# Optimization experiments

Hardware: AMD Instinct MI355X
Metric: run time of the kernel (lower is better)

The kernel has to match this reference:

```python
import jax, jax.numpy as jnp
import numpy as np

POOL_SIZES = (1, 3, 6, 8)
EPS = 1e-5


def conv1x1(x, W, b):
    # x: [b, cin, h, w], W: [cout, cin], b: [cout]
    return jnp.einsum('bchw,oc->bohw', x, W) + b[None, :, None, None]


def ppm(x):
    # x: [b, c, h, w] -> [b, c, S] with S = sum(p*p); H,W divisible by each p
    b, c, h, w = x.shape
    outs = []
    for p in POOL_SIZES:
        pooled = x.reshape(b, c, p, h // p, p, w // p).mean(axis=(3, 5))
        outs.append(pooled.reshape(b, c, p * p))
    return jnp.concatenate(outs, axis=-1)


def setup_inputs() -> dict:
    key = jax.random.key(0)
    ks = jax.random.split(key, 8)
    B, Cin, H, W = 4, 512, 120, 120
    Ck, Cv, Cout = 256, 256, 512
    x = jax.random.normal(ks[0], (B, Cin, H, W), dtype=jnp.float32)
    sc = lambda cin: 1.0 / np.sqrt(cin)
    Wk = jax.random.normal(ks[1], (Ck, Cin), dtype=jnp.float32) * sc(Cin)
    bk = jnp.zeros((Ck,), jnp.float32)
    gamma = jnp.ones((Ck,), jnp.float32)
    beta = jnp.zeros((Ck,), jnp.float32)
    mean = jax.random.normal(ks[2], (Ck,), dtype=jnp.float32) * 0.1
    var = jax.random.uniform(ks[3], (Ck,), dtype=jnp.float32, minval=0.5, maxval=1.5)
    Wv = jax.random.normal(ks[4], (Cv, Cin), dtype=jnp.float32) * sc(Cin)
    bv = jnp.zeros((Cv,), jnp.float32)
    # original inits Conv_Out to zero; use random weights for a nontrivial baseline
    Wo = jax.random.normal(ks[5], (Cout, Cv), dtype=jnp.float32) * sc(Cv)
    bo = jnp.zeros((Cout,), jnp.float32)
    return {'x': x, 'Wk': Wk, 'bk': bk, 'gamma': gamma, 'beta': beta,
            'mean': mean, 'var': var, 'Wv': Wv, 'bv': bv, 'Wo': Wo, 'bo': bo}


def reference(x, Wk, bk, gamma, beta, mean, var, Wv, bv, Wo, bo):
    b, _, h, w = x.shape
    ck = Wk.shape[0]
    cv = Wv.shape[0]
    # shared Conv_Key / Conv_Query: conv1x1 -> BN (inference) -> ReLU
    kq = conv1x1(x, Wk, bk)
    inv = gamma / jnp.sqrt(var + EPS)
    kq = jax.nn.relu(kq * inv[None, :, None, None] + (beta - mean * inv)[None, :, None, None])
    value = ppm(conv1x1(x, Wv, bv)).transpose(0, 2, 1)      # [b, S, cv]
    key = ppm(kq)                                            # [b, ck, S]
    query = kq.reshape(b, ck, h * w).transpose(0, 2, 1)      # [b, hw, ck]
    scores = jnp.einsum('bnc,bcs->bns', query, key) * (ck ** -0.5)
    attn = jax.nn.softmax(scores, axis=-1)                   # [b, hw, S]
    agg = jnp.einsum('bns,bsv->bnv', attn, value)            # [b, hw, cv]
    agg = agg.transpose(0, 2, 1).reshape(b, cv, h, w)
    return conv1x1(agg, Wo, bo)
```

## Files before the change

kernel.cpp:

```cpp
#include <hip/hip_runtime.h>
#include <cstdint>
#include <cstddef>

#define HW 14400
#define WIDTH 120
#define S_TOT 110

typedef unsigned short u16;
typedef __attribute__((ext_vector_type(8))) short bf16x8;
typedef __attribute__((ext_vector_type(4))) float f32x4;

__device__ __forceinline__ u16 f2bf(float x) {
  unsigned u = __float_as_uint(x);
  unsigned r = (u + 0x7fffu + ((u >> 16) & 1u)) >> 16;
  return (u16)r;
}
__device__ __forceinline__ float bf2f(u16 h) {
  return __uint_as_float((unsigned)h << 16);
}

__device__ __forceinline__ void async16(void* lds, const void* g) {
  __builtin_amdgcn_global_load_lds(
      (const __attribute__((address_space(1))) void*)g,
      (__attribute__((address_space(3))) void*)lds, 16, 0, 0);
}

__global__ __launch_bounds__(256) void pool_kernel(const float* __restrict__ in,
                                                   float* __restrict__ outp) {
  __shared__ float part[576];
  const float* plane = in + (size_t)blockIdx.x * HW;
  int t = threadIdx.x;
  for (int bb = t; bb < 576; bb += 256) {
    int by = bb / 24, bx = bb % 24;
    const float* p0 = plane + (by * 5) * WIDTH + bx * 5;
    float s = 0.f;
#pragma unroll
    for (int yy = 0; yy < 5; ++yy)
#pragma unroll
      for (int xx = 0; xx < 5; ++xx) s += p0[yy * WIDTH + xx];
    part[bb] = s;
  }
  __syncthreads();
  if (t < S_TOT) {
    float s = 0.f;
    if (t == 0) {
      for (int i = 0; i < 576; ++i) s += part[i];
      s *= (1.f / 14400.f);
    } else if (t < 10) {
      int idx = t - 1, i = idx / 3, j = idx % 3;
      for (int a = 0; a < 8; ++a)
        for (int c = 0; c < 8; ++c) s += part[(i * 8 + a) * 24 + (j * 8 + c)];
      s *= (1.f / 1600.f);
    } else if (t < 46) {
      int idx = t - 10, i = idx / 6, j = idx % 6;
      for (int a = 0; a < 4; ++a)
        for (int c = 0; c < 4; ++c) s += part[(i * 4 + a) * 24 + (j * 4 + c)];
      s *= (1.f / 400.f);
    } else {
      int idx = t - 46, i = idx / 8, j = idx % 8;
      for (int a = 0; a < 3; ++a)
        for (int c = 0; c < 3; ++c) s += part[(i * 3 + a) * 24 + (j * 3 + c)];
      s *= (1.f / 225.f);
    }
    outp[(size_t)blockIdx.x * S_TOT + t] = s;
  }
}

__global__ __launch_bounds__(256) void convert_w(const float* __restrict__ in,
                                                 u16* __restrict__ hi,
                                                 u16* __restrict__ lo, int n) {
  int i = blockIdx.x * 256 + threadIdx.x;
  if (i < n) {
    float v = in[i];
    u16 h = f2bf(v);
    hi[i] = h;
    lo[i] = f2bf(v - bf2f(h));
  }
}

template <int CIN>
__global__ __launch_bounds__(256) void convert_t(const float* __restrict__ X,
                                                 u16* __restrict__ xth,
                                                 u16* __restrict__ xtl) {
  __shared__ float ls[64][65];
  int b = blockIdx.z;
  int n0 = blockIdx.x * 64, k0 = blockIdx.y * 64;
  int t = threadIdx.x;
  int rt = t >> 4, c4 = (t & 15) * 4;
#pragma unroll
  for (int rr = 0; rr < 4; ++rr) {
    int kk = rr * 16 + rt;
    float4 v = *(const float4*)&X[((size_t)(b * CIN + k0 + kk)) * HW + n0 + c4];
    ls[kk][c4] = v.x; ls[kk][c4 + 1] = v.y; ls[kk][c4 + 2] = v.z; ls[kk][c4 + 3] = v.w;
  }
  __syncthreads();
#pragma unroll
  for (int rr = 0; rr < 4; ++rr) {
    int nn = rr * 16 + rt;
    float v0 = ls[c4 + 0][nn], v1 = ls[c4 + 1][nn], v2 = ls[c4 + 2][nn], v3 = ls[c4 + 3][nn];
    ushort4 oh, ol;
    oh.x = f2bf(v0); ol.x = f2bf(v0 - bf2f(oh.x));
    oh.y = f2bf(v1); ol.y = f2bf(v1 - bf2f(oh.y));
    oh.z = f2bf(v2); ol.z = f2bf(v2 - bf2f(oh.z));
    oh.w = f2bf(v3); ol.w = f2bf(v3 - bf2f(oh.w));
    size_t idx = ((size_t)(b * HW + n0 + nn)) * CIN + k0 + c4;
    *(ushort4*)&xth[idx] = oh;
    *(ushort4*)&xtl[idx] = ol;
  }
}

template <int K, int M_TOT, bool BNRELU>
__global__ __launch_bounds__(512, 2) void gemm_mfma(
    const u16* __restrict__ Ah, const u16* __restrict__ Al,
    const u16* __restrict__ Bh, const u16* __restrict__ Bl,
    float* __restrict__ C,
    const float* __restrict__ p0, const float* __restrict__ p1,
    const float* __restrict__ p2, const float* __restrict__ p3,
    const float* __restrict__ p4) {
  constexpr int NSTEP = K / 32;
  __shared__ alignas(16) u16 sA[3][16][512];
  __shared__ alignas(16) u16 sB[3][24][512];

  int t = threadIdx.x, w = t >> 6, l = t & 63;
  int wm = w >> 2, wn = w & 3;
  int b = blockIdx.z;
  int n0 = blockIdx.x * 192;
  int m0 = blockIdx.y * 128;

  int fr = l & 15, fkc = l >> 4;
  const size_t bOff = (size_t)b * HW;

  auto stage = [&](int ks, int slot) {
    int k0 = ks * 32;
#pragma unroll
    for (int c = 0; c < 5; ++c) {
      int i = w * 5 + c;
      const u16* g;
      u16* d;
      if (i < 8) {
        g = Ah + (size_t)(m0 + i * 16 + fr) * K + k0 + fkc * 8;
        d = &sA[slot][i][0];
      } else if (i < 16) {
        g = Al + (size_t)(m0 + (i - 8) * 16 + fr) * K + k0 + fkc * 8;
        d = &sA[slot][i][0];
      } else if (i < 28) {
        g = Bh + (bOff + n0 + (i - 16) * 16 + fr) * (size_t)K + k0 + fkc * 8;
        d = &sB[slot][i - 16][0];
      } else {
        g = Bl + (bOff + n0 + (i - 28) * 16 + fr) * (size_t)K + k0 + fkc * 8;
        d = &sB[slot][i - 16][0];
      }
      async16(d, g);
    }
  };

  f32x4 acc[4][3];
#pragma unroll
  for (int i = 0; i < 4; ++i)
#pragma unroll
    for (int j = 0; j < 3; ++j) acc[i][j] = (f32x4){0.f, 0.f, 0.f, 0.f};

  stage(0, 0);
  stage(1, 1);

  for (int ks = 0; ks < NSTEP; ++ks) {
    if (ks + 1 < NSTEP)
      asm volatile("s_waitcnt vmcnt(5)" ::: "memory");
    else
      asm volatile("s_waitcnt vmcnt(0)" ::: "memory");
    __builtin_amdgcn_s_barrier();
    __builtin_amdgcn_sched_barrier(0);

    if (ks + 2 < NSTEP) stage(ks + 2, (ks + 2) % 3);

    int cur = ks % 3;
    bf16x8 bh[3], bl[3];
#pragma unroll
    for (int nt = 0; nt < 3; ++nt) {
      bh[nt] = *(const bf16x8*)&sB[cur][wn * 3 + nt][l * 8];
      bl[nt] = *(const bf16x8*)&sB[cur][12 + wn * 3 + nt][l * 8];
    }
    bf16x8 ah[4], al[4];
#pragma unroll
    for (int mt = 0; mt < 4; ++mt) {
      ah[mt] = *(const bf16x8*)&sA[cur][wm * 4 + mt][l * 8];
      al[mt] = *(const bf16x8*)&sA[cur][8 + wm * 4 + mt][l * 8];
    }
    __builtin_amdgcn_s_setprio(1);
#pragma unroll
    for (int mt = 0; mt < 4; ++mt)
#pragma unroll
      for (int nt = 0; nt < 3; ++nt) {
        acc[mt][nt] = __builtin_amdgcn_mfma_f32_16x16x32_bf16(ah[mt], bh[nt], acc[mt][nt], 0, 0, 0);
        acc[mt][nt] = __builtin_amdgcn_mfma_f32_16x16x32_bf16(ah[mt], bl[nt], acc[mt][nt], 0, 0, 0);
        acc[mt][nt] = __builtin_amdgcn_mfma_f32_16x16x32_bf16(al[mt], bh[nt], acc[mt][nt], 0, 0, 0);
      }
    __builtin_amdgcn_s_setprio(0);
  }

#pragma unroll
  for (int mt = 0; mt < 4; ++mt) {
    int mb = m0 + (wm * 4 + mt) * 16 + (l >> 4) * 4;
    float iv[4], ad[4];
    if (BNRELU) {
      float4 g0 = *(const float4*)&p0[mb];
      float4 g1 = *(const float4*)&p1[mb];
      float4 g2 = *(const float4*)&p2[mb];
      float4 g3 = *(const float4*)&p3[mb];
      float4 g4 = *(const float4*)&p4[mb];
      iv[0] = g1.x * rsqrtf(g4.x + 1e-5f);
      iv[1] = g1.y * rsqrtf(g4.y + 1e-5f);
      iv[2] = g1.z * rsqrtf(g4.z + 1e-5f);
      iv[3] = g1.w * rsqrtf(g4.w + 1e-5f);
      ad[0] = (g0.x - g3.x) * iv[0] + g2.x;
      ad[1] = (g0.y - g3.y) * iv[1] + g2.y;
      ad[2] = (g0.z - g3.z) * iv[2] + g2.z;
      ad[3] = (g0.w - g3.w) * iv[3] + g2.w;
    } else {
      float4 g0 = *(const float4*)&p0[mb];
      ad[0] = g0.x; ad[1] = g0.y; ad[2] = g0.z; ad[3] = g0.w;
    }
#pragma unroll
    for (int nt = 0; nt < 3; ++nt) {
      int n = n0 + (wn * 3 + nt) * 16 + fr;
#pragma unroll
      for (int r = 0; r < 4; ++r) {
        float v = acc[mt][nt][r];
        if (BNRELU)
          v = fmaxf(v * iv[r] + ad[r], 0.f);
        else
          v = v + ad[r];
        C[((size_t)(b * M_TOT) + mb + r) * HW + n] = v;
      }
    }
  }
}

__global__ __launch_bounds__(256) void value_kernel(
    const float* __restrict__ Wv, const float* __restrict__ xp,
    const float* __restrict__ bv, u16* __restrict__ vth,
    u16* __restrict__ vtl) {
  int b = blockIdx.x >> 7, s = blockIdx.x & 127;
  int t = threadIdx.x;
  size_t o = ((size_t)(b * 256 + t)) * 128 + s;
  if (s >= S_TOT) { vth[o] = 0; vtl[o] = 0; return; }
  __shared__ float xs[512];
  for (int i = t; i < 512; i += 256) xs[i] = xp[((size_t)b * 512 + i) * S_TOT + s];
  __syncthreads();
  float accv = 0.f;
  const float* wv = Wv + (size_t)t * 512;
  for (int k = 0; k < 512; k += 4) {
    float4 w4 = *(const float4*)&wv[k];
    accv += w4.x * xs[k] + w4.y * xs[k + 1] + w4.z * xs[k + 2] + w4.w * xs[k + 3];
  }
  accv += bv[t];
  u16 h = f2bf(accv);
  vth[o] = h;
  vtl[o] = f2bf(accv - bf2f(h));
}

__global__ __launch_bounds__(256) void convert_key(const float* __restrict__ keyp,
                                                   u16* __restrict__ kth,
                                                   u16* __restrict__ ktl) {
  int b = blockIdx.x;
  int t = threadIdx.x;
  for (int i = t; i < 128 * 256; i += 256) {
    int s = i >> 8, c = i & 255;
    float v = (s < S_TOT) ? keyp[((size_t)(b * 256 + c)) * S_TOT + s] : 0.f;
    u16 h = f2bf(v);
    size_t o = ((size_t)(b * 128 + s)) * 256 + c;
    kth[o] = h;
    ktl[o] = f2bf(v - bf2f(h));
  }
}

__global__ __launch_bounds__(256) void attn_mfma(
    const u16* __restrict__ qh, const u16* __restrict__ ql,
    const u16* __restrict__ kh, const u16* __restrict__ kl,
    const u16* __restrict__ vh, const u16* __restrict__ vl,
    u16* __restrict__ aggh, u16* __restrict__ aggl) {
  __shared__ alignas(16) u16 lds[17408];
  int b = blockIdx.y, pix0 = blockIdx.x * 64;
  int t = threadIdx.x, w = t >> 6, l = t & 63;
  int fr = l & 15, q = l >> 4;

  const u16* kbase_h = kh + (size_t)b * 128 * 256;
  const u16* kbase_l = kl + (size_t)b * 128 * 256;

  f32x4 acc[8];
#pragma unroll
  for (int st = 0; st < 8; ++st) acc[st] = (f32x4){0.f, 0.f, 0.f, 0.f};

  const u16* qbh = qh + ((size_t)(b * HW + pix0 + w * 16 + fr)) * 256 + q * 8;
  const u16* qbl = ql + ((size_t)(b * HW + pix0 + w * 16 + fr)) * 256 + q * 8;

  auto stageK = [&](int ks, int buf) {
    int c0 = ks * 32;
#pragma unroll
    for (int j = 0; j < 4; ++j) {
      int i = t + j * 256;
      int half = i >> 9;
      int idx = i & 511;
      int st = idx >> 6, ll = idx & 63;
      const u16* src = (half ? kbase_l : kbase_h) +
                       (st * 16 + (ll & 15)) * 256 + c0 + (ll >> 4) * 8;
      async16(&lds[buf * 8192 + half * 4096 + idx * 8], src);
    }
  };

  stageK(0, 0);
  for (int ks = 0; ks < 8; ++ks) {
    __syncthreads();
    if (ks < 7) stageK(ks + 1, (ks + 1) & 1);
    bf16x8 ah = *(const bf16x8*)(qbh + ks * 32);
    bf16x8 al = *(const bf16x8*)(qbl + ks * 32);
    const u16* kb = &lds[(ks & 1) * 8192 + l * 8];
#pragma unroll
    for (int st = 0; st < 8; ++st) {
      bf16x8 bh = *(const bf16x8*)(kb + st * 512);
      bf16x8 bl = *(const bf16x8*)(kb + 4096 + st * 512);
      acc[st] = __builtin_amdgcn_mfma_f32_16x16x32_bf16(ah, bh, acc[st], 0, 0, 0);
      acc[st] = __builtin_amdgcn_mfma_f32_16x16x32_bf16(ah, bl, acc[st], 0, 0, 0);
      acc[st] = __builtin_amdgcn_mfma_f32_16x16x32_bf16(al, bh, acc[st], 0, 0, 0);
    }
  }

#pragma unroll
  for (int st = 0; st < 8; ++st)
#pragma unroll
    for (int r = 0; r < 4; ++r) acc[st][r] *= 0.0625f;
  if (fr >= 14) {
#pragma unroll
    for (int r = 0; r < 4; ++r) acc[6][r] = -1e30f;
  }
#pragma unroll
  for (int r = 0; r < 4; ++r) acc[7][r] = -1e30f;

#pragma unroll
  for (int r = 0; r < 4; ++r) {
    float m = -1e30f;
#pragma unroll
    for (int st = 0; st < 8; ++st) m = fmaxf(m, acc[st][r]);
    m = fmaxf(m, __shfl_xor(m, 1));
    m = fmaxf(m, __shfl_xor(m, 2));
    m = fmaxf(m, __shfl_xor(m, 4));
    m = fmaxf(m, __shfl_xor(m, 8));
    float s = 0.f;
#pragma unroll
    for (int st = 0; st < 8; ++st) {
      float e = __expf(acc[st][r] - m);
      acc[st][r] = e;
      s += e;
    }
    s += __shfl_xor(s, 1);
    s += __shfl_xor(s, 2);
    s += __shfl_xor(s, 4);
    s += __shfl_xor(s, 8);
    float inv = 1.f / s;
#pragma unroll
    for (int st = 0; st < 8; ++st) acc[st][r] *= inv;
  }

  __syncthreads();

  int prow = w * 16 + q * 4;
#pragma unroll
  for (int st = 0; st < 8; ++st) {
    int s = st * 16 + fr;
#pragma unroll
    for (int r = 0; r < 4; ++r) {
      float v = acc[st][r];
      u16 h = f2bf(v);
      lds[(prow + r) * 136 + s] = h;
      lds[8704 + (prow + r) * 136 + s] = f2bf(v - bf2f(h));
    }
  }
  __syncthreads();

  f32x4 oacc[4][4];
#pragma unroll
  for (int nt = 0; nt < 4; ++nt)
#pragma unroll
    for (int pt = 0; pt < 4; ++pt) oacc[nt][pt] = (f32x4){0.f, 0.f, 0.f, 0.f};

  const u16* vbh = vh + ((size_t)(b * 256 + w * 64 + fr)) * 128 + q * 8;
  const u16* vbl = vl + ((size_t)(b * 256 + w * 64 + fr)) * 128 + q * 8;

#pragma unroll
  for (int kc = 0; kc < 4; ++kc) {
    bf16x8 ph[4], pl[4];
#pragma unroll
    for (int pt = 0; pt < 4; ++pt) {
      ph[pt] = *(const bf16x8*)&lds[(pt * 16 + fr) * 136 + kc * 32 + q * 8];
      pl[pt] = *(const bf16x8*)&lds[8704 + (pt * 16 + fr) * 136 + kc * 32 + q * 8];
    }
#pragma unroll
    for (int nt = 0; nt < 4; ++nt) {
      bf16x8 a_h = *(const bf16x8*)(vbh + (size_t)nt * 16 * 128 + kc * 32);
      bf16x8 a_l = *(const bf16x8*)(vbl + (size_t)nt * 16 * 128 + kc * 32);
#pragma unroll
      for (int pt = 0; pt < 4; ++pt) {
        oacc[nt][pt] = __builtin_amdgcn_mfma_f32_16x16x32_bf16(a_h, ph[pt], oacc[nt][pt], 0, 0, 0);
        oacc[nt][pt] = __builtin_amdgcn_mfma_f32_16x16x32_bf16(a_h, pl[pt], oacc[nt][pt], 0, 0, 0);
        oacc[nt][pt] = __builtin_amdgcn_mfma_f32_16x16x32_bf16(a_l, ph[pt], oacc[nt][pt], 0, 0, 0);
      }
    }
  }

#pragma unroll
  for (int nt = 0; nt < 4; ++nt) {
#pragma unroll
    for (int pt = 0; pt < 4; ++pt) {
      ushort4 oh, ol;
      float v0 = oacc[nt][pt][0], v1 = oacc[nt][pt][1];
      float v2 = oacc[nt][pt][2], v3 = oacc[nt][pt][3];
      oh.x = f2bf(v0); ol.x = f2bf(v0 - bf2f(oh.x));
      oh.y = f2bf(v1); ol.y = f2bf(v1 - bf2f(oh.y));
      oh.z = f2bf(v2); ol.z = f2bf(v2 - bf2f(oh.z));
      oh.w = f2bf(v3); ol.w = f2bf(v3 - bf2f(oh.w));
      size_t o = ((size_t)(b * HW + pix0 + pt * 16 + fr)) * 256 + (w * 4 + nt) * 16 + q * 4;
      *(ushort4*)&aggh[o] = oh;
      *(ushort4*)&aggl[o] = ol;
    }
  }
}

extern "C" void kernel_launch(void* const* d_in, const int* in_sizes, int n_in,
                              void* d_out, int out_size, void* d_ws, size_t ws_size,
                              hipStream_t stream) {
  (void)in_sizes; (void)n_in; (void)out_size; (void)ws_size;
  const float* x     = (const float*)d_in[0];
  const float* Wk    = (const float*)d_in[1];
  const float* bk    = (const float*)d_in[2];
  const float* gamma = (const float*)d_in[3];
  const float* beta  = (const float*)d_in[4];
  const float* mean  = (const float*)d_in[5];
  const float* var   = (const float*)d_in[6];
  const float* Wv    = (const float*)d_in[7];
  const float* bv    = (const float*)d_in[8];
  const float* Wo    = (const float*)d_in[9];
  const float* bo    = (const float*)d_in[10];
  float* out = (float*)d_out;

  char* p = (char*)d_ws;
  float* kq = (float*)p;      p += (size_t)14745600 * 4;
  u16* xth = (u16*)p;         p += (size_t)29491200 * 2;
  u16* xtl = (u16*)p;         p += (size_t)29491200 * 2;
  u16* wkh = (u16*)p;         p += 131072 * 2;
  u16* wkl = (u16*)p;         p += 131072 * 2;
  u16* woh = (u16*)p;         p += 131072 * 2;
  u16* wol = (u16*)p;         p += 131072 * 2;
  float* xp = (float*)p;      p += (size_t)4 * 512 * 110 * 4;
  float* keyp = (float*)p;    p += (size_t)4 * 256 * 110 * 4;
  u16* vth = (u16*)p;         p += (size_t)4 * 256 * 128 * 2;
  u16* vtl = (u16*)p;         p += (size_t)4 * 256 * 128 * 2;
  u16* kth = (u16*)p;         p += (size_t)4 * 128 * 256 * 2;
  u16* ktl = (u16*)p;         p += (size_t)4 * 128 * 256 * 2;
  u16* aggh = xth;
  u16* kqth = xth + (size_t)14745600;
  u16* aggl = xtl;
  u16* kqtl = xtl + (size_t)14745600;

  convert_w<<<512, 256, 0, stream>>>(Wk, wkh, wkl, 256 * 512);
  convert_w<<<512, 256, 0, stream>>>(Wo, woh, wol, 512 * 256);
  convert_t<512><<<dim3(225, 8, 4), 256, 0, stream>>>(x, xth, xtl);
  pool_kernel<<<dim3(4 * 512), dim3(256), 0, stream>>>(x, xp);
  value_kernel<<<dim3(4 * 128), dim3(256), 0, stream>>>(Wv, xp, bv, vth, vtl);
  gemm_mfma<512, 256, true><<<dim3(75, 2, 4), 512, 0, stream>>>(
      wkh, wkl, xth, xtl, kq, bk, gamma, beta, mean, var);
  convert_t<256><<<dim3(225, 4, 4), 256, 0, stream>>>(kq, kqth, kqtl);
  pool_kernel<<<dim3(4 * 256), dim3(256), 0, stream>>>(kq, keyp);
  convert_key<<<dim3(4), dim3(256), 0, stream>>>(keyp, kth, ktl);
  attn_mfma<<<dim3(225, 4), 256, 0, stream>>>(kqth, kqtl, kth, ktl, vth, vtl,
                                              aggh, aggl);
  gemm_mfma<256, 512, false><<<dim3(75, 4, 4), 512, 0, stream>>>(
      woh, wol, aggh, aggl, out, bo, nullptr, nullptr, nullptr, nullptr);
}
```

Before: 560.0 us.

## Fuse kq transpose/bf16 split into key GEMM epilogue; separable pooling sums

The BN+ReLU key GEMM epilogue now also writes the transposed bf16 hi/lo split of kq through a padded LDS staging buffer, which removes the separate convert_t pass over kq when the workspace is large enough. Shared memory is merged into one flat array so the epilogue can reuse it after a barrier. The pool kernel first computes 5-row column sums and then sums 5 columns, cutting redundant global loads. The fused path needs about 59 MB more workspace and falls back to the old kernel if that is not available; the extra epilogue stores may add register pressure and stall the GEMM tail.

```diff
diff --git a/kernel.cpp b/kernel.cpp
--- a/kernel.cpp
+++ b/kernel.cpp
@@ -27,18 +27,20 @@
 
 __global__ __launch_bounds__(256) void pool_kernel(const float* __restrict__ in,
                                                    float* __restrict__ outp) {
+  __shared__ float colsum[2880];
   __shared__ float part[576];
   const float* plane = in + (size_t)blockIdx.x * HW;
   int t = threadIdx.x;
+  for (int i = t; i < 2880; i += 256) {
+    int by = i / 120, x = i - by * 120;
+    const float* p0 = plane + (by * 5) * WIDTH + x;
+    colsum[i] = p0[0] + p0[WIDTH] + p0[2 * WIDTH] + p0[3 * WIDTH] + p0[4 * WIDTH];
+  }
+  __syncthreads();
   for (int bb = t; bb < 576; bb += 256) {
-    int by = bb / 24, bx = bb % 24;
-    const float* p0 = plane + (by * 5) * WIDTH + bx * 5;
-    float s = 0.f;
-#pragma unroll
-    for (int yy = 0; yy < 5; ++yy)
-#pragma unroll
-      for (int xx = 0; xx < 5; ++xx) s += p0[yy * WIDTH + xx];
-    part[bb] = s;
+    int by = bb / 24, bx = bb - by * 24;
+    const float* c = &colsum[by * 120 + bx * 5];
+    part[bb] = c[0] + c[1] + c[2] + c[3] + c[4];
   }
   __syncthreads();
   if (t < S_TOT) {
@@ -116,10 +118,10 @@
     float* __restrict__ C,
     const float* __restrict__ p0, const float* __restrict__ p1,
     const float* __restrict__ p2, const float* __restrict__ p3,
-    const float* __restrict__ p4) {
+    const float* __restrict__ p4,
+    u16* __restrict__ Th, u16* __restrict__ Tl) {
   constexpr int NSTEP = K / 32;
-  __shared__ alignas(16) u16 sA[3][16][512];
-  __shared__ alignas(16) u16 sB[3][24][512];
+  __shared__ alignas(16) u16 smem[61440];
 
   int t = threadIdx.x, w = t >> 6, l = t & 63;
   int wm = w >> 2, wn = w & 3;
@@ -139,16 +141,16 @@
       u16* d;
       if (i < 8) {
         g = Ah + (size_t)(m0 + i * 16 + fr) * K + k0 + fkc * 8;
-        d = &sA[slot][i][0];
+        d = &smem[slot * 8192 + i * 512];
       } else if (i < 16) {
         g = Al + (size_t)(m0 + (i - 8) * 16 + fr) * K + k0 + fkc * 8;
-        d = &sA[slot][i][0];
+        d = &smem[slot * 8192 + i * 512];
       } else if (i < 28) {
         g = Bh + (bOff + n0 + (i - 16) * 16 + fr) * (size_t)K + k0 + fkc * 8;
-        d = &sB[slot][i - 16][0];
+        d = &smem[24576 + slot * 12288 + (i - 16) * 512];
       } else {
         g = Bl + (bOff + n0 + (i - 28) * 16 + fr) * (size_t)K + k0 + fkc * 8;
-        d = &sB[slot][i - 16][0];
+        d = &smem[24576 + slot * 12288 + (i - 16) * 512];
       }
       async16(d, g);
     }
@@ -177,14 +179,14 @@
     bf16x8 bh[3], bl[3];
 #pragma unroll
     for (int nt = 0; nt < 3; ++nt) {
-      bh[nt] = *(const bf16x8*)&sB[cur][wn * 3 + nt][l * 8];
-      bl[nt] = *(const bf16x8*)&sB[cur][12 + wn * 3 + nt][l * 8];
+      bh[nt] = *(const bf16x8*)&smem[24576 + cur * 12288 + (wn * 3 + nt) * 512 + l * 8];
+      bl[nt] = *(const bf16x8*)&smem[24576 + cur * 12288 + (12 + wn * 3 + nt) * 512 + l * 8];
     }
     bf16x8 ah[4], al[4];
 #pragma unroll
     for (int mt = 0; mt < 4; ++mt) {
-      ah[mt] = *(const bf16x8*)&sA[cur][wm * 4 + mt][l * 8];
-      al[mt] = *(const bf16x8*)&sA[cur][8 + wm * 4 + mt][l * 8];
+      ah[mt] = *(const bf16x8*)&smem[cur * 8192 + (wm * 4 + mt) * 512 + l * 8];
+      al[mt] = *(const bf16x8*)&smem[cur * 8192 + (8 + wm * 4 + mt) * 512 + l * 8];
     }
     __builtin_amdgcn_s_setprio(1);
 #pragma unroll
@@ -198,9 +200,12 @@
     __builtin_amdgcn_s_setprio(0);
   }
 
+  __syncthreads();
+
+  int q4 = (l >> 4) * 4;
 #pragma unroll
   for (int mt = 0; mt < 4; ++mt) {
-    int mb = m0 + (wm * 4 + mt) * 16 + (l >> 4) * 4;
+    int mb = m0 + (wm * 4 + mt) * 16 + q4;
     float iv[4], ad[4];
     if (BNRELU) {
       float4 g0 = *(const float4*)&p0[mb];
@@ -223,15 +228,35 @@
 #pragma unroll
     for (int nt = 0; nt < 3; ++nt) {
       int n = n0 + (wn * 3 + nt) * 16 + fr;
+      float v[4];
 #pragma unroll
       for (int r = 0; r < 4; ++r) {
-        float v = acc[mt][nt][r];
-        if (BNRELU)
-          v = fmaxf(v * iv[r] + ad[r], 0.f);
-        else
-          v = v + ad[r];
-        C[((size_t)(b * M_TOT) + mb + r) * HW + n] = v;
+        float x = acc[mt][nt][r];
+        v[r] = BNRELU ? fmaxf(x * iv[r] + ad[r], 0.f) : x + ad[r];
+        C[((size_t)(b * M_TOT) + mb + r) * HW + n] = v[r];
       }
+      if (BNRELU && Th) {
+        ushort4 hh, ll;
+        hh.x = f2bf(v[0]); ll.x = f2bf(v[0] - bf2f(hh.x));
+        hh.y = f2bf(v[1]); ll.y = f2bf(v[1] - bf2f(hh.y));
+        hh.z = f2bf(v[2]); ll.z = f2bf(v[2] - bf2f(hh.z));
+        hh.w = f2bf(v[3]); ll.w = f2bf(v[3] - bf2f(hh.w));
+        int nl = (wn * 3 + nt) * 16 + fr;
+        int ml = (wm * 4 + mt) * 16 + q4;
+        *(ushort4*)&smem[nl * 136 + ml] = hh;
+        *(ushort4*)&smem[26112 + nl * 136 + ml] = ll;
+      }
+    }
+  }
+  if (BNRELU && Th) {
+    __syncthreads();
+#pragma unroll
+    for (int it = 0; it < 6; ++it) {
+      int row = it * 32 + (t >> 4);
+      int c8 = (t & 15) * 8;
+      size_t go = (bOff + n0 + row) * (size_t)M_TOT + m0 + c8;
+      *(bf16x8*)&Th[go] = *(const bf16x8*)&smem[row * 136 + c8];
+      *(bf16x8*)&Tl[go] = *(const bf16x8*)&smem[26112 + row * 136 + c8];
     }
   }
 }
@@ -428,7 +453,7 @@
 extern "C" void kernel_launch(void* const* d_in, const int* in_sizes, int n_in,
                               void* d_out, int out_size, void* d_ws, size_t ws_size,
                               hipStream_t stream) {
-  (void)in_sizes; (void)n_in; (void)out_size; (void)ws_size;
+  (void)in_sizes; (void)n_in; (void)out_size;
   const float* x     = (const float*)d_in[0];
   const float* Wk    = (const float*)d_in[1];
   const float* bk    = (const float*)d_in[2];
@@ -456,10 +481,14 @@
   u16* vtl = (u16*)p;         p += (size_t)4 * 256 * 128 * 2;
   u16* kth = (u16*)p;         p += (size_t)4 * 128 * 256 * 2;
   u16* ktl = (u16*)p;         p += (size_t)4 * 128 * 256 * 2;
+  u16* kqth_f = (u16*)p;      p += (size_t)14745600 * 2;
+  u16* kqtl_f = (u16*)p;      p += (size_t)14745600 * 2;
+  bool fused = ((size_t)(p - (char*)d_ws) <= ws_size);
+
   u16* aggh = xth;
-  u16* kqth = xth + (size_t)14745600;
   u16* aggl = xtl;
-  u16* kqtl = xtl + (size_t)14745600;
+  u16* kqth = fused ? kqth_f : xth + (size_t)14745600;
+  u16* kqtl = fused ? kqtl_f : xtl + (size_t)14745600;
 
   convert_w<<<512, 256, 0, stream>>>(Wk, wkh, wkl, 256 * 512);
   convert_w<<<512, 256, 0, stream>>>(Wo, woh, wol, 512 * 256);
@@ -467,12 +496,15 @@
   pool_kernel<<<dim3(4 * 512), dim3(256), 0, stream>>>(x, xp);
   value_kernel<<<dim3(4 * 128), dim3(256), 0, stream>>>(Wv, xp, bv, vth, vtl);
   gemm_mfma<512, 256, true><<<dim3(75, 2, 4), 512, 0, stream>>>(
-      wkh, wkl, xth, xtl, kq, bk, gamma, beta, mean, var);
-  convert_t<256><<<dim3(225, 4, 4), 256, 0, stream>>>(kq, kqth, kqtl);
+      wkh, wkl, xth, xtl, kq, bk, gamma, beta, mean, var,
+      fused ? kqth : (u16*)nullptr, fused ? kqtl : (u16*)nullptr);
+  if (!fused)
+    convert_t<256><<<dim3(225, 4, 4), 256, 0, stream>>>(kq, kqth, kqtl);
   pool_kernel<<<dim3(4 * 256), dim3(256), 0, stream>>>(kq, keyp);
   convert_key<<<dim3(4), dim3(256), 0, stream>>>(keyp, kth, ktl);
   attn_mfma<<<dim3(225, 4), 256, 0, stream>>>(kqth, kqtl, kth, ktl, vth, vtl,
                                               aggh, aggl);
   gemm_mfma<256, 512, false><<<dim3(75, 4, 4), 512, 0, stream>>>(
-      woh, wol, aggh, aggl, out, bo, nullptr, nullptr, nullptr, nullptr);
-}
+      woh, wol, aggh, aggl, out, bo, nullptr, nullptr, nullptr, nullptr,
+      nullptr, nullptr);
+}
```

New measurement: 557.3 us. No clear change (-0.5%).
